# Kernel tuning notes

Hardware: AMD Instinct MI355X
Metric: run time of the kernel (lower is better)

Reference implementation:

```python
import jax, jax.numpy as jnp
import numpy as np

HIDDEN = 128
NUM_RADIAL = 16
NUM_DENSE = 3
OUT_DIM = 1
N_NODES = 50000
N_EDGES = 600000


def setup_inputs() -> dict:
    key = jax.random.key(0)
    ks = jax.random.split(key, 16)
    h = jax.random.normal(ks[0], (N_NODES, HIDDEN), dtype=jnp.float32)
    radial_basis = jax.random.normal(ks[1], (N_EDGES, NUM_RADIAL), dtype=jnp.float32)
    edge_index = jax.random.randint(ks[2], (2, N_EDGES), 0, N_NODES, dtype=jnp.int32)

    def lin(k, fan_in, fan_out):
        bound = 1.0 / np.sqrt(fan_in)
        kw, kb = jax.random.split(k)
        W = jax.random.uniform(kw, (fan_in, fan_out), minval=-bound, maxval=bound, dtype=jnp.float32)
        b = jax.random.uniform(kb, (fan_out,), minval=-bound, maxval=bound, dtype=jnp.float32)
        return W, b

    rW1, rb1 = lin(ks[3], NUM_RADIAL, HIDDEN)
    rW2, rb2 = lin(ks[4], HIDDEN, HIDDEN)
    dW, db = [], []
    for i in range(NUM_DENSE):
        W, b = lin(ks[5 + i], HIDDEN, HIDDEN)
        dW.append(W); db.append(b)
    oW, ob = lin(ks[10], HIDDEN, OUT_DIM)
    return {
        "h": h, "radial_basis": radial_basis, "edge_index": edge_index,
        "rW1": rW1, "rb1": rb1, "rW2": rW2, "rb2": rb2,
        "dW0": dW[0], "db0": db[0], "dW1": dW[1], "db1": db[1], "dW2": dW[2], "db2": db[2],
        "oW": oW, "ob": ob,
    }


def reference(h, radial_basis, edge_index, rW1, rb1, rW2, rb2,
              dW0, db0, dW1, db1, dW2, db2, oW, ob):
    src, dst = edge_index[0], edge_index[1]
    # radial_net: Linear -> SiLU -> Linear, output [n_edges, hidden]
    W = jax.nn.silu(radial_basis @ rW1 + rb1) @ rW2 + rb2
    # gather -> multiply -> scatter-add (message passing)
    h_edge = h[src] * W                      # [n_edges, hidden]
    x = jax.ops.segment_sum(h_edge, dst, num_segments=h.shape[0])  # [n_atoms, hidden]
    # dense layers
    for dw, dbias in ((dW0, db0), (dW1, db1), (dW2, db2)):
        x = jax.nn.silu(x @ dw + dbias)
    return x @ oW + ob                        # [n_atoms, output_dim]
```

## Files before the change

### kernel.cpp

```cpp
#include <hip/hip_runtime.h>

typedef short bf16x8 __attribute__((ext_vector_type(8)));
typedef float f32x4 __attribute__((ext_vector_type(4)));
typedef float f32x2 __attribute__((ext_vector_type(2)));
typedef unsigned int u32x4 __attribute__((ext_vector_type(4)));

__device__ __forceinline__ unsigned short f2bf(float f) {
  unsigned int u = __float_as_uint(f);
  u = (u + 0x7FFFu + ((u >> 16) & 1u)) >> 16;
  return (unsigned short)u;
}
__device__ __forceinline__ float bf2f(unsigned short u) {
  return __uint_as_float(((unsigned int)u) << 16);
}
__device__ __forceinline__ float silu_f(float v) {
  return v * (1.0f / (1.0f + __expf(-v)));
}
__device__ __forceinline__ unsigned int pkbf(float a, float b) {
  unsigned int r;
  asm("v_cvt_pk_bf16_f32 %0, %1, %2" : "=v"(r) : "v"(a), "v"(b));
  return r;
}
__device__ __forceinline__ void st2bf(char* base, int byA, int byB, float a, float b) {
  unsigned int p = pkbf(a, b);
  *(unsigned short*)(base + byA) = (unsigned short)p;
  *(unsigned short*)(base + byB) = (unsigned short)(p >> 16);
}

__global__ void k_prep(const float* __restrict__ rW1, const float* __restrict__ rb1,
                       const float* __restrict__ rW2, const float* __restrict__ dW0,
                       const float* __restrict__ dW1, const float* __restrict__ dW2,
                       unsigned short* __restrict__ wb) {
  int i = blockIdx.x * blockDim.x + threadIdx.x;
  if (i < 4096) {
    int j = i & 7, lane = (i >> 3) & 63, nt = i >> 9;
    int k = (lane >> 4) * 8 + j, n = nt * 16 + (lane & 15);
    float v = (k < 16) ? rW1[k * 128 + n] : (k == 16 ? rb1[n] : 0.0f);
    wb[i] = f2bf(v);
  } else if (i < 4096 + 4 * 16384) {
    int i2 = i - 4096, buf = i2 >> 14, r = i2 & 16383;
    int j = r & 7, lane = (r >> 3) & 63, g = r >> 9, kc = g & 3, nt = g >> 2;
    int k = kc * 32 + (lane >> 4) * 8 + j, n = nt * 16 + (lane & 15);
    const float* W = (buf == 0) ? rW2 : (buf == 1) ? dW0 : (buf == 2) ? dW1 : dW2;
    wb[4096 + buf * 16384 + r] = f2bf(W[k * 128 + n]);
  }
}

__global__ void k_hist(const int* __restrict__ ei, int* __restrict__ hist, int E) {
  int e = blockIdx.x * blockDim.x + threadIdx.x;
  if (e < E) atomicAdd(&hist[ei[E + e]], 1);
}

__global__ __launch_bounds__(1024) void k_scanA(const int* __restrict__ hist,
                                                int* __restrict__ part, int N) {
  __shared__ int red[1024];
  const int t = threadIdx.x;
  const int i = blockIdx.x * 1024 + t;
  red[t] = (i < N) ? hist[i] : 0;
  __syncthreads();
  for (int o = 512; o; o >>= 1) {
    if (t < o) red[t] += red[t + o];
    __syncthreads();
  }
  if (t == 0) part[blockIdx.x] = red[0];
}

__global__ __launch_bounds__(1024) void k_scanC(
    const int* __restrict__ hist, const int* __restrict__ part,
    int* __restrict__ row_start, int* __restrict__ bump, int N, int nb) {
  __shared__ int sh[1024];
  __shared__ int s_off;
  const int t = threadIdx.x;
  const int b = blockIdx.x;
  if (t < 64) {
    int p = (t < nb) ? part[t] : 0;
#pragma unroll
    for (int o = 1; o < 64; o <<= 1) {
      int u = __shfl_up(p, o);
      if (t >= o) p += u;
    }
    if (b == 0) {
      if (t == 0) s_off = 0;
    } else if (t == b - 1) {
      s_off = p;
    }
  }
  __syncthreads();
  const int i = b * 1024 + t;
  const int v = (i < N) ? hist[i] : 0;
  sh[t] = v;
  __syncthreads();
  for (int o = 1; o < 1024; o <<= 1) {
    int u = (t >= o) ? sh[t - o] : 0;
    __syncthreads();
    sh[t] += u;
    __syncthreads();
  }
  const int excl = s_off + sh[t] - v;
  if (i < N) {
    row_start[i] = excl;
    bump[i] = excl;
  } else if (i == N) {
    row_start[N] = excl;
  }
}

__global__ void k_pos(const int* __restrict__ ei, int* __restrict__ bump,
                      int* __restrict__ pos, int E) {
  int e = blockIdx.x * blockDim.x + threadIdx.x;
  if (e < E) pos[e] = atomicAdd(&bump[ei[E + e]], 1);
}

__global__ __launch_bounds__(256, 2) void k_edge2(
    const float* __restrict__ rb, const int* __restrict__ ei,
    const float* __restrict__ h, const unsigned short* __restrict__ B1,
    const unsigned short* __restrict__ B2, const float* __restrict__ rb2,
    const int* __restrict__ pos, unsigned short* __restrict__ Mbuf,
    int E, int ntiles) {
  const int lane = threadIdx.x & 63;
  const int wid = threadIdx.x >> 6;
  const int kg = lane >> 4;
  const int c15 = lane & 15;
  __shared__ __align__(16) unsigned short hid[64 * 128];

  bf16x8 b2f[8][4];
#pragma unroll
  for (int nt = 0; nt < 8; ++nt)
#pragma unroll
    for (int kc = 0; kc < 4; ++kc)
      b2f[nt][kc] = *(const bf16x8*)(B2 + (((nt * 4 + kc) * 64 + lane) << 3));

  float rb2r[8];
#pragma unroll
  for (int nt = 0; nt < 8; ++nt) rb2r[nt] = rb2[nt * 16 + c15];

  for (int t = blockIdx.x; t < ntiles; t += gridDim.x) {
    const int ebase = t * 64 + wid * 16;

    bf16x8 a1 = {};
    if (kg < 2) {
      const int e = ebase + c15;
      if (e < E) {
        const f32x4 v0 = __builtin_nontemporal_load((const f32x4*)(rb + (size_t)e * 16 + kg * 8));
        const f32x4 v1 = __builtin_nontemporal_load((const f32x4*)(rb + (size_t)e * 16 + kg * 8 + 4));
        unsigned int p0 = pkbf(v0[0], v0[1]), p1 = pkbf(v0[2], v0[3]);
        unsigned int p2 = pkbf(v1[0], v1[1]), p3 = pkbf(v1[2], v1[3]);
        a1[0] = (short)(p0 & 0xffff); a1[1] = (short)(p0 >> 16);
        a1[2] = (short)(p1 & 0xffff); a1[3] = (short)(p1 >> 16);
        a1[4] = (short)(p2 & 0xffff); a1[5] = (short)(p2 >> 16);
        a1[6] = (short)(p3 & 0xffff); a1[7] = (short)(p3 >> 16);
      }
    } else if (kg == 2) {
      a1[0] = (short)0x3F80;
    }

#pragma unroll
    for (int nt = 0; nt < 8; ++nt) {
      bf16x8 b1 = *(const bf16x8*)(B1 + ((nt * 64 + lane) << 3));
      f32x4 d1 = {};
      d1 = __builtin_amdgcn_mfma_f32_16x16x32_bf16(a1, b1, d1, 0, 0, 0);
#pragma unroll
      for (int r = 0; r < 4; r += 2) {
        const int row0 = wid * 16 + kg * 4 + r;
        const int row1 = row0 + 1;
        const int col2 = (nt * 16 + c15) * 2;
        st2bf((char*)hid,
              (row0 * 256 + col2) ^ ((row0 & 7) << 4),
              (row1 * 256 + col2) ^ ((row1 & 7) << 4),
              silu_f(d1[r]), silu_f(d1[r + 1]));
      }
    }

    const int arow = wid * 16 + c15;
    f32x4 acc[8] = {};
#pragma unroll
    for (int kc = 0; kc < 4; ++kc) {
      int byt = arow * 256 + (kc * 32 + kg * 8) * 2;
      byt ^= (arow & 7) << 4;
      const bf16x8 a2 = *(const bf16x8*)((const char*)hid + byt);
#pragma unroll
      for (int nt = 0; nt < 8; ++nt)
        acc[nt] = __builtin_amdgcn_mfma_f32_16x16x32_bf16(a2, b2f[nt][kc], acc[nt], 0, 0, 0);
    }

#pragma unroll
    for (int nt = 0; nt < 8; ++nt)
#pragma unroll
      for (int r = 0; r < 4; r += 2) {
        const int row0 = wid * 16 + kg * 4 + r;
        const int row1 = row0 + 1;
        const int col2 = (nt * 16 + c15) * 2;
        st2bf((char*)hid,
              (row0 * 256 + col2) ^ ((row0 & 7) << 4),
              (row1 * 256 + col2) ^ ((row1 & 7) << 4),
              acc[nt][r] + rb2r[nt], acc[nt][r + 1] + rb2r[nt]);
      }

#pragma unroll
    for (int pass = 0; pass < 2; ++pass) {
      const int ro = wid * 16 + pass * 8 + (lane >> 3);
      const int e = t * 64 + ro;
      if (e < E) {
        const int p = pos[e];
        const int s = ei[e];
        const int cg = (lane & 7) * 16;
        const int swz = (ro & 7) << 4;
        const int bas = ro * 256 + cg * 2;
        const bf16x8 w0 = *(const bf16x8*)((const char*)hid + (bas ^ swz));
        const bf16x8 w1 = *(const bf16x8*)((const char*)hid + ((bas + 16) ^ swz));
        const f32x4* hp = (const f32x4*)(h + (size_t)s * 128 + cg);
        const f32x4 h0 = hp[0], h1 = hp[1], h2 = hp[2], h3 = hp[3];
        u32x4 m0, m1;
        m0[0] = pkbf(bf2f((unsigned short)w0[0]) * h0[0], bf2f((unsigned short)w0[1]) * h0[1]);
        m0[1] = pkbf(bf2f((unsigned short)w0[2]) * h0[2], bf2f((unsigned short)w0[3]) * h0[3]);
        m0[2] = pkbf(bf2f((unsigned short)w0[4]) * h1[0], bf2f((unsigned short)w0[5]) * h1[1]);
        m0[3] = pkbf(bf2f((unsigned short)w0[6]) * h1[2], bf2f((unsigned short)w0[7]) * h1[3]);
        m1[0] = pkbf(bf2f((unsigned short)w1[0]) * h2[0], bf2f((unsigned short)w1[1]) * h2[1]);
        m1[1] = pkbf(bf2f((unsigned short)w1[2]) * h2[2], bf2f((unsigned short)w1[3]) * h2[3]);
        m1[2] = pkbf(bf2f((unsigned short)w1[4]) * h3[0], bf2f((unsigned short)w1[5]) * h3[1]);
        m1[3] = pkbf(bf2f((unsigned short)w1[6]) * h3[2], bf2f((unsigned short)w1[7]) * h3[3]);
        *(u32x4*)(Mbuf + (size_t)p * 128 + cg) = m0;
        *(u32x4*)(Mbuf + (size_t)p * 128 + cg + 8) = m1;
      }
    }
  }
}

__global__ __launch_bounds__(256) void k_gather2(
    const unsigned short* __restrict__ Mbuf, const int* __restrict__ row_start,
    float* __restrict__ x, int NN) {
  const int lane = threadIdx.x & 63;
  const int r4 = lane >> 4;
  const int c16 = lane & 15;
  const int wv = (int)((blockIdx.x * blockDim.x + threadIdx.x) >> 6);
  const int nw = (int)((gridDim.x * blockDim.x) >> 6);
  for (int n = wv; n < NN; n += nw) {
    const int b0 = row_start[n], b1 = row_start[n + 1];
    float sa[8] = {}, sb[8] = {};
    int j = b0 + r4;
    for (; j + 4 < b1; j += 8) {
      const bf16x8 va = *(const bf16x8*)(Mbuf + (size_t)j * 128 + c16 * 8);
      const bf16x8 vb = *(const bf16x8*)(Mbuf + (size_t)(j + 4) * 128 + c16 * 8);
#pragma unroll
      for (int k = 0; k < 8; ++k) {
        sa[k] += bf2f((unsigned short)va[k]);
        sb[k] += bf2f((unsigned short)vb[k]);
      }
    }
    if (j < b1) {
      const bf16x8 va = *(const bf16x8*)(Mbuf + (size_t)j * 128 + c16 * 8);
#pragma unroll
      for (int k = 0; k < 8; ++k) sa[k] += bf2f((unsigned short)va[k]);
    }
#pragma unroll
    for (int k = 0; k < 8; ++k) {
      float s = sa[k] + sb[k];
      s += __shfl_xor(s, 16);
      s += __shfl_xor(s, 32);
      sa[k] = s;
    }
    if (r4 == 0) {
      f32x4 o0 = {sa[0], sa[1], sa[2], sa[3]};
      f32x4 o1 = {sa[4], sa[5], sa[6], sa[7]};
      *(f32x4*)(x + (size_t)n * 128 + c16 * 8) = o0;
      *(f32x4*)(x + (size_t)n * 128 + c16 * 8 + 4) = o1;
    }
  }
}

__device__ __forceinline__ void dense_silu_layer(
    unsigned short* xt, const unsigned short* __restrict__ W,
    const float* __restrict__ bias, int wid, int kg, int c15, int lane) {
  const int arow = wid * 16 + c15;
  f32x4 acc[8] = {};
#pragma unroll
  for (int kc = 0; kc < 4; ++kc) {
    int byt = arow * 256 + (kc * 32 + kg * 8) * 2;
    byt ^= (arow & 7) << 4;
    const bf16x8 a2 = *(const bf16x8*)((const char*)xt + byt);
#pragma unroll
    for (int nt = 0; nt < 8; ++nt) {
      const bf16x8 bf = *(const bf16x8*)(W + (((nt * 4 + kc) * 64 + lane) << 3));
      acc[nt] = __builtin_amdgcn_mfma_f32_16x16x32_bf16(a2, bf, acc[nt], 0, 0, 0);
    }
  }
#pragma unroll
  for (int nt = 0; nt < 8; ++nt) {
    const float b = bias[nt * 16 + c15];
#pragma unroll
    for (int r = 0; r < 4; r += 2) {
      const int row0 = wid * 16 + kg * 4 + r;
      const int row1 = row0 + 1;
      const int col2 = (nt * 16 + c15) * 2;
      st2bf((char*)xt,
            (row0 * 256 + col2) ^ ((row0 & 7) << 4),
            (row1 * 256 + col2) ^ ((row1 & 7) << 4),
            silu_f(acc[nt][r] + b), silu_f(acc[nt][r + 1] + b));
    }
  }
}

__global__ __launch_bounds__(256) void k_tile(
    const float* __restrict__ x, const unsigned short* __restrict__ Dw,
    const float* __restrict__ db0, const float* __restrict__ db1,
    const float* __restrict__ db2, const float* __restrict__ oW,
    const float* __restrict__ ob, float* __restrict__ out, int NN, int tiles) {
  const int lane = threadIdx.x & 63;
  const int wid = threadIdx.x >> 6;
  const int kg = lane >> 4;
  const int c15 = lane & 15;
  __shared__ __align__(16) unsigned short xt[64 * 128];

  for (int t = blockIdx.x; t < tiles; t += gridDim.x) {
    const int nbase = t * 64 + wid * 16;

#pragma unroll
    for (int i = 0; i < 16; ++i) {
      const int n = nbase + i;
      const int row = wid * 16 + i;
      f32x2 v = {};
      if (n < NN) v = *(const f32x2*)(x + (size_t)n * 128 + lane * 2);
      const int byt = (row * 256 + lane * 4) ^ ((row & 7) << 4);
      *(unsigned int*)((char*)xt + byt) = pkbf(v[0], v[1]);
    }

    dense_silu_layer(xt, Dw, db0, wid, kg, c15, lane);
    dense_silu_layer(xt, Dw + 16384, db1, wid, kg, c15, lane);

    {
      const int arow = wid * 16 + c15;
      const unsigned short* W = Dw + 32768;
      f32x4 acc[8] = {};
#pragma unroll
      for (int kc = 0; kc < 4; ++kc) {
        int byt = arow * 256 + (kc * 32 + kg * 8) * 2;
        byt ^= (arow & 7) << 4;
        const bf16x8 a2 = *(const bf16x8*)((const char*)xt + byt);
#pragma unroll
        for (int nt = 0; nt < 8; ++nt) {
          const bf16x8 bf = *(const bf16x8*)(W + (((nt * 4 + kc) * 64 + lane) << 3));
          acc[nt] = __builtin_amdgcn_mfma_f32_16x16x32_bf16(a2, bf, acc[nt], 0, 0, 0);
        }
      }
      const float obv = ob[0];
#pragma unroll
      for (int r = 0; r < 4; ++r) {
        float p = 0.f;
#pragma unroll
        for (int nt = 0; nt < 8; ++nt) {
          const float b = db2[nt * 16 + c15];
          p += silu_f(acc[nt][r] + b) * oW[nt * 16 + c15];
        }
        p += __shfl_xor(p, 1);
        p += __shfl_xor(p, 2);
        p += __shfl_xor(p, 4);
        p += __shfl_xor(p, 8);
        const int n = nbase + kg * 4 + r;
        if (c15 == 0 && n < NN) out[n] = p + obv;
      }
    }
  }
}

__global__ __launch_bounds__(256, 2) void k_edge(
    const float* __restrict__ rb, const int* __restrict__ ei,
    const float* __restrict__ h, const unsigned short* __restrict__ B1,
    const unsigned short* __restrict__ B2, const float* __restrict__ rb2,
    float* __restrict__ x, int E, int ntiles) {
  const int lane = threadIdx.x & 63;
  const int wid = threadIdx.x >> 6;
  const int kg = lane >> 4;
  const int c15 = lane & 15;
  __shared__ __align__(16) unsigned short hid[64 * 128];

  bf16x8 b2f[8][4];
#pragma unroll
  for (int nt = 0; nt < 8; ++nt)
#pragma unroll
    for (int kc = 0; kc < 4; ++kc)
      b2f[nt][kc] = *(const bf16x8*)(B2 + (((nt * 4 + kc) * 64 + lane) << 3));

  float rb2r[8];
#pragma unroll
  for (int nt = 0; nt < 8; ++nt) rb2r[nt] = rb2[nt * 16 + c15];

  for (int t = blockIdx.x; t < ntiles; t += gridDim.x) {
    const int ebase = t * 64 + wid * 16;
    bf16x8 a1 = {};
    if (kg < 2) {
      const int e = ebase + c15;
      if (e < E) {
        const f32x4 v0 = *(const f32x4*)(rb + (size_t)e * 16 + kg * 8);
        const f32x4 v1 = *(const f32x4*)(rb + (size_t)e * 16 + kg * 8 + 4);
        a1[0] = (short)f2bf(v0[0]); a1[1] = (short)f2bf(v0[1]);
        a1[2] = (short)f2bf(v0[2]); a1[3] = (short)f2bf(v0[3]);
        a1[4] = (short)f2bf(v1[0]); a1[5] = (short)f2bf(v1[1]);
        a1[6] = (short)f2bf(v1[2]); a1[7] = (short)f2bf(v1[3]);
      }
    } else if (kg == 2) {
      a1[0] = (short)0x3F80;
    }
#pragma unroll
    for (int nt = 0; nt < 8; ++nt) {
      bf16x8 b1 = *(const bf16x8*)(B1 + ((nt * 64 + lane) << 3));
      f32x4 d1 = {};
      d1 = __builtin_amdgcn_mfma_f32_16x16x32_bf16(a1, b1, d1, 0, 0, 0);
#pragma unroll
      for (int r = 0; r < 4; ++r) {
        const int row = wid * 16 + kg * 4 + r;
        int byt = row * 256 + (nt * 16 + c15) * 2;
        byt ^= (row & 7) << 4;
        *(unsigned short*)((char*)hid + byt) = f2bf(silu_f(d1[r]));
      }
    }
    const int arow = wid * 16 + c15;
    f32x4 acc[8] = {};
#pragma unroll
    for (int kc = 0; kc < 4; ++kc) {
      int byt = arow * 256 + (kc * 32 + kg * 8) * 2;
      byt ^= (arow & 7) << 4;
      const bf16x8 a2 = *(const bf16x8*)((const char*)hid + byt);
#pragma unroll
      for (int nt = 0; nt < 8; ++nt)
        acc[nt] = __builtin_amdgcn_mfma_f32_16x16x32_bf16(a2, b2f[nt][kc], acc[nt], 0, 0, 0);
    }
#pragma unroll
    for (int r = 0; r < 4; ++r) {
      const int e = ebase + kg * 4 + r;
      if (e < E) {
        const int s = ei[e];
        const int d = ei[E + e];
#pragma unroll
        for (int nt = 0; nt < 8; ++nt) {
          const int col = nt * 16 + c15;
          const float w = acc[nt][r] + rb2r[nt];
          const float hv = h[(size_t)s * 128 + col];
          atomicAdd(x + (size_t)d * 128 + col, w * hv);
        }
      }
    }
  }
}

__global__ __launch_bounds__(256, 2) void k_dense(
    float* __restrict__ x, const unsigned short* __restrict__ Bw,
    const float* __restrict__ bias, int M) {
  const int lane = threadIdx.x & 63;
  const int wid = threadIdx.x >> 6;
  const int kg = lane >> 4;
  const int c15 = lane & 15;

  bf16x8 bf[8][4];
#pragma unroll
  for (int nt = 0; nt < 8; ++nt)
#pragma unroll
    for (int kc = 0; kc < 4; ++kc)
      bf[nt][kc] = *(const bf16x8*)(Bw + (((nt * 4 + kc) * 64 + lane) << 3));

  float br[8];
#pragma unroll
  for (int nt = 0; nt < 8; ++nt) br[nt] = bias[nt * 16 + c15];

  const int tiles = (M + 63) >> 6;
  for (int t = blockIdx.x; t < tiles; t += gridDim.x) {
    const int rbase = t * 64 + wid * 16;
    const int row = rbase + c15;
    bf16x8 a[4];
#pragma unroll
    for (int kc = 0; kc < 4; ++kc) {
      bf16x8 az = {};
      if (row < M) {
        const f32x4 v0 = *(const f32x4*)(x + (size_t)row * 128 + kc * 32 + kg * 8);
        const f32x4 v1 = *(const f32x4*)(x + (size_t)row * 128 + kc * 32 + kg * 8 + 4);
        az[0] = (short)f2bf(v0[0]); az[1] = (short)f2bf(v0[1]);
        az[2] = (short)f2bf(v0[2]); az[3] = (short)f2bf(v0[3]);
        az[4] = (short)f2bf(v1[0]); az[5] = (short)f2bf(v1[1]);
        az[6] = (short)f2bf(v1[2]); az[7] = (short)f2bf(v1[3]);
      }
      a[kc] = az;
    }
    f32x4 acc[8] = {};
#pragma unroll
    for (int kc = 0; kc < 4; ++kc)
#pragma unroll
      for (int nt = 0; nt < 8; ++nt)
        acc[nt] = __builtin_amdgcn_mfma_f32_16x16x32_bf16(a[kc], bf[nt][kc], acc[nt], 0, 0, 0);
#pragma unroll
    for (int r = 0; r < 4; ++r) {
      const int orow = rbase + kg * 4 + r;
      if (orow < M) {
#pragma unroll
        for (int nt = 0; nt < 8; ++nt)
          x[(size_t)orow * 128 + nt * 16 + c15] = silu_f(acc[nt][r] + br[nt]);
      }
    }
  }
}

__global__ void k_out(const float* __restrict__ x, const float* __restrict__ oW,
                      const float* __restrict__ ob, float* __restrict__ out, int M) {
  const int lane = threadIdx.x & 63;
  const int w = (int)((blockIdx.x * blockDim.x + threadIdx.x) >> 6);
  const int nw = (int)((gridDim.x * blockDim.x) >> 6);
  const float w0 = oW[lane], w1 = oW[64 + lane];
  const float obv = ob[0];
  for (int row = w; row < M; row += nw) {
    float a = x[(size_t)row * 128 + lane] * w0 + x[(size_t)row * 128 + 64 + lane] * w1;
#pragma unroll
    for (int m = 32; m; m >>= 1) a += __shfl_xor(a, m);
    if (lane == 0) out[row] = a + obv;
  }
}

extern "C" void kernel_launch(void* const* d_in, const int* in_sizes, int n_in,
                              void* d_out, int out_size, void* d_ws, size_t ws_size,
                              hipStream_t stream) {
  const float* h   = (const float*)d_in[0];
  const float* rb  = (const float*)d_in[1];
  const int*   ei  = (const int*)d_in[2];
  const float* rW1 = (const float*)d_in[3];
  const float* rb1 = (const float*)d_in[4];
  const float* rW2 = (const float*)d_in[5];
  const float* rb2 = (const float*)d_in[6];
  const float* dW0 = (const float*)d_in[7];
  const float* db0 = (const float*)d_in[8];
  const float* dW1 = (const float*)d_in[9];
  const float* db1 = (const float*)d_in[10];
  const float* dW2 = (const float*)d_in[11];
  const float* db2 = (const float*)d_in[12];
  const float* oW  = (const float*)d_in[13];
  const float* ob  = (const float*)d_in[14];

  const int NN = in_sizes[0] / 128;
  const int E  = in_sizes[1] / 16;

  char* base = (char*)d_ws;
  size_t off = 0;
  auto alloc = [&](size_t bytes) {
    char* p = base + off;
    off += (bytes + 255) & ~(size_t)255;
    return p;
  };
  float* x            = (float*)alloc((size_t)NN * 128 * 4);
  unsigned short* wb  = (unsigned short*)alloc((size_t)69632 * 2);
  int* row_start      = (int*)alloc((size_t)(NN + 1) * 4);
  int* hist           = (int*)alloc((size_t)NN * 4);
  int* bump           = (int*)alloc((size_t)NN * 4);
  int* part           = (int*)alloc((size_t)64 * 4);
  int* pos            = (int*)alloc((size_t)E * 4);
  unsigned short* Mb  = (unsigned short*)alloc((size_t)E * 256);
  const bool fits = off <= ws_size && NN <= 65535;

  k_prep<<<(69632 + 255) / 256, 256, 0, stream>>>(rW1, rb1, rW2, dW0, dW1, dW2, wb);

  const int ntiles = (E + 63) / 64;
  const int gE = (E + 255) / 256;

  if (fits) {
    hipMemsetAsync(hist, 0, (size_t)NN * 4, stream);
    k_hist<<<gE, 256, 0, stream>>>(ei, hist, E);
    k_scanA<<<64, 1024, 0, stream>>>(hist, part, NN);
    k_scanC<<<64, 1024, 0, stream>>>(hist, part, row_start, bump, NN, 64);
    k_pos<<<gE, 256, 0, stream>>>(ei, bump, pos, E);
    const int eg = ntiles < 2048 ? ntiles : 2048;
    k_edge2<<<eg, 256, 0, stream>>>(rb, ei, h, wb, wb + 4096, rb2, pos, Mb, E, ntiles);
    k_gather2<<<(NN + 3) / 4, 256, 0, stream>>>(Mb, row_start, x, NN);
    const int tiles = (NN + 63) / 64;
    k_tile<<<tiles, 256, 0, stream>>>(x, wb + 20480, db0, db1, db2,
                                      oW, ob, (float*)d_out, NN, tiles);
  } else {
    hipMemsetAsync(x, 0, (size_t)NN * 512, stream);
    const int eg = ntiles < 1024 ? ntiles : 1024;
    k_edge<<<eg, 256, 0, stream>>>(rb, ei, h, wb, wb + 4096, rb2, x, E, ntiles);
    k_dense<<<512, 256, 0, stream>>>(x, wb + 20480, db0, NN);
    k_dense<<<512, 256, 0, stream>>>(x, wb + 36864, db1, NN);
    k_dense<<<512, 256, 0, stream>>>(x, wb + 53248, db2, NN);
    k_out<<<512, 256, 0, stream>>>(x, oW, ob, (float*)d_out, NN);
  }
}
```

Baseline: 315.5 us.

## Sort edges by destination and reduce messages in-tile instead of via buffer

Edges are now sorted by destination into an (edge, src, dst) array, and the edge kernel processes the sorted slots. Messages are kept in shared memory and segment-reduced per tile, so only interior segments are written directly and tile-boundary segments use atomics into x. This removes the E×256-byte bf16 message buffer round trip and the separate gather kernel, at the cost of random reads of radial_basis by original edge id, a memset of x, and float atomics at segment boundaries. The grid is now one block per tile instead of a persistent loop, so B2 fragments are reloaded per tile.

```diff
diff --git a/kernel.cpp b/kernel.cpp
--- a/kernel.cpp
+++ b/kernel.cpp
@@ -67,7 +67,7 @@
 
 __global__ __launch_bounds__(1024) void k_scanC(
     const int* __restrict__ hist, const int* __restrict__ part,
-    int* __restrict__ row_start, int* __restrict__ bump, int N, int nb) {
+    int* __restrict__ bump, int N, int nb) {
   __shared__ int sh[1024];
   __shared__ int s_off;
   const int t = threadIdx.x;
@@ -96,32 +96,39 @@
     sh[t] += u;
     __syncthreads();
   }
-  const int excl = s_off + sh[t] - v;
-  if (i < N) {
-    row_start[i] = excl;
-    bump[i] = excl;
-  } else if (i == N) {
-    row_start[N] = excl;
-  }
-}
-
-__global__ void k_pos(const int* __restrict__ ei, int* __restrict__ bump,
-                      int* __restrict__ pos, int E) {
+  if (i < N) bump[i] = s_off + sh[t] - v;
+}
+
+__global__ void k_pos2(const int* __restrict__ ei, int* __restrict__ bump,
+                       int4* __restrict__ esd, int E) {
   int e = blockIdx.x * blockDim.x + threadIdx.x;
-  if (e < E) pos[e] = atomicAdd(&bump[ei[E + e]], 1);
-}
-
-__global__ __launch_bounds__(256, 2) void k_edge2(
-    const float* __restrict__ rb, const int* __restrict__ ei,
-    const float* __restrict__ h, const unsigned short* __restrict__ B1,
-    const unsigned short* __restrict__ B2, const float* __restrict__ rb2,
-    const int* __restrict__ pos, unsigned short* __restrict__ Mbuf,
-    int E, int ntiles) {
-  const int lane = threadIdx.x & 63;
-  const int wid = threadIdx.x >> 6;
+  if (e < E) {
+    const int s = ei[e];
+    const int d = ei[E + e];
+    const int p = atomicAdd(&bump[d], 1);
+    esd[p] = make_int4(e, s, d, 0);
+  }
+}
+
+__global__ __launch_bounds__(256, 2) void k_edge3(
+    const float* __restrict__ rb, const float* __restrict__ h,
+    const unsigned short* __restrict__ B1, const unsigned short* __restrict__ B2,
+    const float* __restrict__ rb2, const int4* __restrict__ esd,
+    float* __restrict__ x, int E) {
+  const int tid = threadIdx.x;
+  const int lane = tid & 63;
+  const int wid = tid >> 6;
   const int kg = lane >> 4;
   const int c15 = lane & 15;
   __shared__ __align__(16) unsigned short hid[64 * 128];
+  __shared__ int sdst[64];
+
+  const int tbase = blockIdx.x * 64;
+
+  if (tid < 64) {
+    const int slot = tbase + tid;
+    sdst[tid] = (slot < E) ? esd[slot].z : -1;
+  }
 
   bf16x8 b2f[8][4];
 #pragma unroll
@@ -134,137 +141,112 @@
 #pragma unroll
   for (int nt = 0; nt < 8; ++nt) rb2r[nt] = rb2[nt * 16 + c15];
 
-  for (int t = blockIdx.x; t < ntiles; t += gridDim.x) {
-    const int ebase = t * 64 + wid * 16;
-
-    bf16x8 a1 = {};
-    if (kg < 2) {
-      const int e = ebase + c15;
-      if (e < E) {
-        const f32x4 v0 = __builtin_nontemporal_load((const f32x4*)(rb + (size_t)e * 16 + kg * 8));
-        const f32x4 v1 = __builtin_nontemporal_load((const f32x4*)(rb + (size_t)e * 16 + kg * 8 + 4));
-        unsigned int p0 = pkbf(v0[0], v0[1]), p1 = pkbf(v0[2], v0[3]);
-        unsigned int p2 = pkbf(v1[0], v1[1]), p3 = pkbf(v1[2], v1[3]);
-        a1[0] = (short)(p0 & 0xffff); a1[1] = (short)(p0 >> 16);
-        a1[2] = (short)(p1 & 0xffff); a1[3] = (short)(p1 >> 16);
-        a1[4] = (short)(p2 & 0xffff); a1[5] = (short)(p2 >> 16);
-        a1[6] = (short)(p3 & 0xffff); a1[7] = (short)(p3 >> 16);
-      }
-    } else if (kg == 2) {
-      a1[0] = (short)0x3F80;
-    }
-
-#pragma unroll
-    for (int nt = 0; nt < 8; ++nt) {
-      bf16x8 b1 = *(const bf16x8*)(B1 + ((nt * 64 + lane) << 3));
-      f32x4 d1 = {};
-      d1 = __builtin_amdgcn_mfma_f32_16x16x32_bf16(a1, b1, d1, 0, 0, 0);
-#pragma unroll
-      for (int r = 0; r < 4; r += 2) {
-        const int row0 = wid * 16 + kg * 4 + r;
-        const int row1 = row0 + 1;
-        const int col2 = (nt * 16 + c15) * 2;
-        st2bf((char*)hid,
-              (row0 * 256 + col2) ^ ((row0 & 7) << 4),
-              (row1 * 256 + col2) ^ ((row1 & 7) << 4),
-              silu_f(d1[r]), silu_f(d1[r + 1]));
-      }
-    }
-
-    const int arow = wid * 16 + c15;
-    f32x4 acc[8] = {};
-#pragma unroll
-    for (int kc = 0; kc < 4; ++kc) {
-      int byt = arow * 256 + (kc * 32 + kg * 8) * 2;
-      byt ^= (arow & 7) << 4;
-      const bf16x8 a2 = *(const bf16x8*)((const char*)hid + byt);
-#pragma unroll
-      for (int nt = 0; nt < 8; ++nt)
-        acc[nt] = __builtin_amdgcn_mfma_f32_16x16x32_bf16(a2, b2f[nt][kc], acc[nt], 0, 0, 0);
-    }
-
+  bf16x8 a1 = {};
+  if (kg < 2) {
+    const int slot = tbase + wid * 16 + c15;
+    if (slot < E) {
+      const int eid = esd[slot].x;
+      const f32x4 v0 = __builtin_nontemporal_load((const f32x4*)(rb + (size_t)eid * 16 + kg * 8));
+      const f32x4 v1 = __builtin_nontemporal_load((const f32x4*)(rb + (size_t)eid * 16 + kg * 8 + 4));
+      unsigned int p0 = pkbf(v0[0], v0[1]), p1 = pkbf(v0[2], v0[3]);
+      unsigned int p2 = pkbf(v1[0], v1[1]), p3 = pkbf(v1[2], v1[3]);
+      a1[0] = (short)(p0 & 0xffff); a1[1] = (short)(p0 >> 16);
+      a1[2] = (short)(p1 & 0xffff); a1[3] = (short)(p1 >> 16);
+      a1[4] = (short)(p2 & 0xffff); a1[5] = (short)(p2 >> 16);
+      a1[6] = (short)(p3 & 0xffff); a1[7] = (short)(p3 >> 16);
+    }
+  } else if (kg == 2) {
+    a1[0] = (short)0x3F80;
+  }
+
+#pragma unroll
+  for (int nt = 0; nt < 8; ++nt) {
+    bf16x8 b1 = *(const bf16x8*)(B1 + ((nt * 64 + lane) << 3));
+    f32x4 d1 = {};
+    d1 = __builtin_amdgcn_mfma_f32_16x16x32_bf16(a1, b1, d1, 0, 0, 0);
+#pragma unroll
+    for (int r = 0; r < 4; r += 2) {
+      const int row0 = wid * 16 + kg * 4 + r;
+      const int row1 = row0 + 1;
+      const int col2 = (nt * 16 + c15) * 2;
+      st2bf((char*)hid,
+            (row0 * 256 + col2) ^ ((row0 & 7) << 4),
+            (row1 * 256 + col2) ^ ((row1 & 7) << 4),
+            silu_f(d1[r]), silu_f(d1[r + 1]));
+    }
+  }
+
+  const int arow = wid * 16 + c15;
+  f32x4 acc[8] = {};
+#pragma unroll
+  for (int kc = 0; kc < 4; ++kc) {
+    int byt = arow * 256 + (kc * 32 + kg * 8) * 2;
+    byt ^= (arow & 7) << 4;
+    const bf16x8 a2 = *(const bf16x8*)((const char*)hid + byt);
 #pragma unroll
     for (int nt = 0; nt < 8; ++nt)
-#pragma unroll
-      for (int r = 0; r < 4; r += 2) {
-        const int row0 = wid * 16 + kg * 4 + r;
-        const int row1 = row0 + 1;
-        const int col2 = (nt * 16 + c15) * 2;
-        st2bf((char*)hid,
-              (row0 * 256 + col2) ^ ((row0 & 7) << 4),
-              (row1 * 256 + col2) ^ ((row1 & 7) << 4),
-              acc[nt][r] + rb2r[nt], acc[nt][r + 1] + rb2r[nt]);
-      }
-
-#pragma unroll
-    for (int pass = 0; pass < 2; ++pass) {
-      const int ro = wid * 16 + pass * 8 + (lane >> 3);
-      const int e = t * 64 + ro;
-      if (e < E) {
-        const int p = pos[e];
-        const int s = ei[e];
-        const int cg = (lane & 7) * 16;
-        const int swz = (ro & 7) << 4;
-        const int bas = ro * 256 + cg * 2;
-        const bf16x8 w0 = *(const bf16x8*)((const char*)hid + (bas ^ swz));
-        const bf16x8 w1 = *(const bf16x8*)((const char*)hid + ((bas + 16) ^ swz));
-        const f32x4* hp = (const f32x4*)(h + (size_t)s * 128 + cg);
-        const f32x4 h0 = hp[0], h1 = hp[1], h2 = hp[2], h3 = hp[3];
-        u32x4 m0, m1;
-        m0[0] = pkbf(bf2f((unsigned short)w0[0]) * h0[0], bf2f((unsigned short)w0[1]) * h0[1]);
-        m0[1] = pkbf(bf2f((unsigned short)w0[2]) * h0[2], bf2f((unsigned short)w0[3]) * h0[3]);
-        m0[2] = pkbf(bf2f((unsigned short)w0[4]) * h1[0], bf2f((unsigned short)w0[5]) * h1[1]);
-        m0[3] = pkbf(bf2f((unsigned short)w0[6]) * h1[2], bf2f((unsigned short)w0[7]) * h1[3]);
-        m1[0] = pkbf(bf2f((unsigned short)w1[0]) * h2[0], bf2f((unsigned short)w1[1]) * h2[1]);
-        m1[1] = pkbf(bf2f((unsigned short)w1[2]) * h2[2], bf2f((unsigned short)w1[3]) * h2[3]);
-        m1[2] = pkbf(bf2f((unsigned short)w1[4]) * h3[0], bf2f((unsigned short)w1[5]) * h3[1]);
-        m1[3] = pkbf(bf2f((unsigned short)w1[6]) * h3[2], bf2f((unsigned short)w1[7]) * h3[3]);
-        *(u32x4*)(Mbuf + (size_t)p * 128 + cg) = m0;
-        *(u32x4*)(Mbuf + (size_t)p * 128 + cg + 8) = m1;
-      }
-    }
-  }
-}
-
-__global__ __launch_bounds__(256) void k_gather2(
-    const unsigned short* __restrict__ Mbuf, const int* __restrict__ row_start,
-    float* __restrict__ x, int NN) {
-  const int lane = threadIdx.x & 63;
-  const int r4 = lane >> 4;
-  const int c16 = lane & 15;
-  const int wv = (int)((blockIdx.x * blockDim.x + threadIdx.x) >> 6);
-  const int nw = (int)((gridDim.x * blockDim.x) >> 6);
-  for (int n = wv; n < NN; n += nw) {
-    const int b0 = row_start[n], b1 = row_start[n + 1];
-    float sa[8] = {}, sb[8] = {};
-    int j = b0 + r4;
-    for (; j + 4 < b1; j += 8) {
-      const bf16x8 va = *(const bf16x8*)(Mbuf + (size_t)j * 128 + c16 * 8);
-      const bf16x8 vb = *(const bf16x8*)(Mbuf + (size_t)(j + 4) * 128 + c16 * 8);
-#pragma unroll
-      for (int k = 0; k < 8; ++k) {
-        sa[k] += bf2f((unsigned short)va[k]);
-        sb[k] += bf2f((unsigned short)vb[k]);
-      }
-    }
-    if (j < b1) {
-      const bf16x8 va = *(const bf16x8*)(Mbuf + (size_t)j * 128 + c16 * 8);
-#pragma unroll
-      for (int k = 0; k < 8; ++k) sa[k] += bf2f((unsigned short)va[k]);
-    }
-#pragma unroll
-    for (int k = 0; k < 8; ++k) {
-      float s = sa[k] + sb[k];
-      s += __shfl_xor(s, 16);
-      s += __shfl_xor(s, 32);
-      sa[k] = s;
-    }
-    if (r4 == 0) {
-      f32x4 o0 = {sa[0], sa[1], sa[2], sa[3]};
-      f32x4 o1 = {sa[4], sa[5], sa[6], sa[7]};
-      *(f32x4*)(x + (size_t)n * 128 + c16 * 8) = o0;
-      *(f32x4*)(x + (size_t)n * 128 + c16 * 8 + 4) = o1;
-    }
+      acc[nt] = __builtin_amdgcn_mfma_f32_16x16x32_bf16(a2, b2f[nt][kc], acc[nt], 0, 0, 0);
+  }
+
+#pragma unroll
+  for (int nt = 0; nt < 8; ++nt)
+#pragma unroll
+    for (int r = 0; r < 4; r += 2) {
+      const int row0 = wid * 16 + kg * 4 + r;
+      const int row1 = row0 + 1;
+      const int col2 = (nt * 16 + c15) * 2;
+      st2bf((char*)hid,
+            (row0 * 256 + col2) ^ ((row0 & 7) << 4),
+            (row1 * 256 + col2) ^ ((row1 & 7) << 4),
+            acc[nt][r] + rb2r[nt], acc[nt][r + 1] + rb2r[nt]);
+    }
+
+#pragma unroll
+  for (int pass = 0; pass < 2; ++pass) {
+    const int ro = wid * 16 + pass * 8 + (lane >> 3);
+    const int slot = tbase + ro;
+    if (slot < E) {
+      const int s = esd[slot].y;
+      const int cg = (lane & 7) * 16;
+      const int swz = (ro & 7) << 4;
+      const int bas = ro * 256 + cg * 2;
+      const bf16x8 w0 = *(const bf16x8*)((const char*)hid + (bas ^ swz));
+      const bf16x8 w1 = *(const bf16x8*)((const char*)hid + ((bas + 16) ^ swz));
+      const f32x4* hp = (const f32x4*)(h + (size_t)s * 128 + cg);
+      const f32x4 h0 = hp[0], h1 = hp[1], h2 = hp[2], h3 = hp[3];
+      u32x4 m0, m1;
+      m0[0] = pkbf(bf2f((unsigned short)w0[0]) * h0[0], bf2f((unsigned short)w0[1]) * h0[1]);
+      m0[1] = pkbf(bf2f((unsigned short)w0[2]) * h0[2], bf2f((unsigned short)w0[3]) * h0[3]);
+      m0[2] = pkbf(bf2f((unsigned short)w0[4]) * h1[0], bf2f((unsigned short)w0[5]) * h1[1]);
+      m0[3] = pkbf(bf2f((unsigned short)w0[6]) * h1[2], bf2f((unsigned short)w0[7]) * h1[3]);
+      m1[0] = pkbf(bf2f((unsigned short)w1[0]) * h2[0], bf2f((unsigned short)w1[1]) * h2[1]);
+      m1[1] = pkbf(bf2f((unsigned short)w1[2]) * h2[2], bf2f((unsigned short)w1[3]) * h2[3]);
+      m1[2] = pkbf(bf2f((unsigned short)w1[4]) * h3[0], bf2f((unsigned short)w1[5]) * h3[1]);
+      m1[3] = pkbf(bf2f((unsigned short)w1[6]) * h3[2], bf2f((unsigned short)w1[7]) * h3[3]);
+      *(u32x4*)((char*)hid + (bas ^ swz)) = m0;
+      *(u32x4*)((char*)hid + ((bas + 16) ^ swz)) = m1;
+    }
+  }
+
+  __syncthreads();
+
+  {
+    const int col = tid & 127;
+    const int r0 = (tid >> 7) << 5;
+    float a = 0.f;
+    int prev = sdst[r0];
+    int segstart = r0;
+    for (int row = r0; row < r0 + 32; ++row) {
+      const int d = sdst[row];
+      if (d != prev) {
+        float* xp = x + (size_t)prev * 128 + col;
+        if (segstart == r0) atomicAdd(xp, a); else *xp = a;
+        a = 0.f; prev = d; segstart = row;
+      }
+      const int byt = (row * 256 + col * 2) ^ ((row & 7) << 4);
+      a += bf2f(*(const unsigned short*)((const char*)hid + byt));
+    }
+    if (prev >= 0) atomicAdd(x + (size_t)prev * 128 + col, a);
   }
 }
 
@@ -543,28 +525,26 @@
   };
   float* x            = (float*)alloc((size_t)NN * 128 * 4);
   unsigned short* wb  = (unsigned short*)alloc((size_t)69632 * 2);
-  int* row_start      = (int*)alloc((size_t)(NN + 1) * 4);
   int* hist           = (int*)alloc((size_t)NN * 4);
   int* bump           = (int*)alloc((size_t)NN * 4);
   int* part           = (int*)alloc((size_t)64 * 4);
-  int* pos            = (int*)alloc((size_t)E * 4);
-  unsigned short* Mb  = (unsigned short*)alloc((size_t)E * 256);
+  int4* esd           = (int4*)alloc((size_t)E * 16);
   const bool fits = off <= ws_size && NN <= 65535;
 
   k_prep<<<(69632 + 255) / 256, 256, 0, stream>>>(rW1, rb1, rW2, dW0, dW1, dW2, wb);
 
   const int ntiles = (E + 63) / 64;
   const int gE = (E + 255) / 256;
+  const int nb = (NN + 1023) / 1024;
 
   if (fits) {
     hipMemsetAsync(hist, 0, (size_t)NN * 4, stream);
+    hipMemsetAsync(x, 0, (size_t)NN * 512, stream);
     k_hist<<<gE, 256, 0, stream>>>(ei, hist, E);
-    k_scanA<<<64, 1024, 0, stream>>>(hist, part, NN);
-    k_scanC<<<64, 1024, 0, stream>>>(hist, part, row_start, bump, NN, 64);
-    k_pos<<<gE, 256, 0, stream>>>(ei, bump, pos, E);
-    const int eg = ntiles < 2048 ? ntiles : 2048;
-    k_edge2<<<eg, 256, 0, stream>>>(rb, ei, h, wb, wb + 4096, rb2, pos, Mb, E, ntiles);
-    k_gather2<<<(NN + 3) / 4, 256, 0, stream>>>(Mb, row_start, x, NN);
+    k_scanA<<<nb, 1024, 0, stream>>>(hist, part, NN);
+    k_scanC<<<nb, 1024, 0, stream>>>(hist, part, bump, NN, nb);
+    k_pos2<<<gE, 256, 0, stream>>>(ei, bump, esd, E);
+    k_edge3<<<ntiles, 256, 0, stream>>>(rb, h, wb, wb + 4096, rb2, esd, x, E);
     const int tiles = (NN + 63) / 64;
     k_tile<<<tiles, 256, 0, stream>>>(x, wb + 20480, db0, db1, db2,
                                       oW, ob, (float*)d_out, NN, tiles);
```

Result: slower. 364.7 us (+15.6%).

## Fuse segment gather into dense-tile kernel and fold hist memset into prep

Applied to the files above, without the earlier changes.

Merges the CSR gather-sum kernel into the dense-layer tile kernel, so each 512-thread block sums messages for 128 nodes directly into shared memory as bf16. This drops the fp32 x round-trip through global memory and one kernel launch. It also zeroes the histogram inside k_prep instead of a separate memset and sizes the scan grids from NN. In exchange, the gather now processes two nodes per wave with divergent lengths and adds block-wide syncs before the MFMA layers.

```diff
diff --git a/kernel.cpp b/kernel.cpp
--- a/kernel.cpp
+++ b/kernel.cpp
@@ -30,7 +30,8 @@
 __global__ void k_prep(const float* __restrict__ rW1, const float* __restrict__ rb1,
                        const float* __restrict__ rW2, const float* __restrict__ dW0,
                        const float* __restrict__ dW1, const float* __restrict__ dW2,
-                       unsigned short* __restrict__ wb) {
+                       unsigned short* __restrict__ wb, int* __restrict__ hist,
+                       int nzero) {
   int i = blockIdx.x * blockDim.x + threadIdx.x;
   if (i < 4096) {
     int j = i & 7, lane = (i >> 3) & 63, nt = i >> 9;
@@ -43,6 +44,8 @@
     int k = kc * 32 + (lane >> 4) * 8 + j, n = nt * 16 + (lane & 15);
     const float* W = (buf == 0) ? rW2 : (buf == 1) ? dW0 : (buf == 2) ? dW1 : dW2;
     wb[4096 + buf * 16384 + r] = f2bf(W[k * 128 + n]);
+  } else if (i - 69632 < nzero) {
+    hist[i - 69632] = 0;
   }
 }
 
@@ -226,48 +229,6 @@
   }
 }
 
-__global__ __launch_bounds__(256) void k_gather2(
-    const unsigned short* __restrict__ Mbuf, const int* __restrict__ row_start,
-    float* __restrict__ x, int NN) {
-  const int lane = threadIdx.x & 63;
-  const int r4 = lane >> 4;
-  const int c16 = lane & 15;
-  const int wv = (int)((blockIdx.x * blockDim.x + threadIdx.x) >> 6);
-  const int nw = (int)((gridDim.x * blockDim.x) >> 6);
-  for (int n = wv; n < NN; n += nw) {
-    const int b0 = row_start[n], b1 = row_start[n + 1];
-    float sa[8] = {}, sb[8] = {};
-    int j = b0 + r4;
-    for (; j + 4 < b1; j += 8) {
-      const bf16x8 va = *(const bf16x8*)(Mbuf + (size_t)j * 128 + c16 * 8);
-      const bf16x8 vb = *(const bf16x8*)(Mbuf + (size_t)(j + 4) * 128 + c16 * 8);
-#pragma unroll
-      for (int k = 0; k < 8; ++k) {
-        sa[k] += bf2f((unsigned short)va[k]);
-        sb[k] += bf2f((unsigned short)vb[k]);
-      }
-    }
-    if (j < b1) {
-      const bf16x8 va = *(const bf16x8*)(Mbuf + (size_t)j * 128 + c16 * 8);
-#pragma unroll
-      for (int k = 0; k < 8; ++k) sa[k] += bf2f((unsigned short)va[k]);
-    }
-#pragma unroll
-    for (int k = 0; k < 8; ++k) {
-      float s = sa[k] + sb[k];
-      s += __shfl_xor(s, 16);
-      s += __shfl_xor(s, 32);
-      sa[k] = s;
-    }
-    if (r4 == 0) {
-      f32x4 o0 = {sa[0], sa[1], sa[2], sa[3]};
-      f32x4 o1 = {sa[4], sa[5], sa[6], sa[7]};
-      *(f32x4*)(x + (size_t)n * 128 + c16 * 8) = o0;
-      *(f32x4*)(x + (size_t)n * 128 + c16 * 8 + 4) = o1;
-    }
-  }
-}
-
 __device__ __forceinline__ void dense_silu_layer(
     unsigned short* xt, const unsigned short* __restrict__ W,
     const float* __restrict__ bias, int wid, int kg, int c15, int lane) {
@@ -300,29 +261,77 @@
   }
 }
 
-__global__ __launch_bounds__(256) void k_tile(
-    const float* __restrict__ x, const unsigned short* __restrict__ Dw,
-    const float* __restrict__ db0, const float* __restrict__ db1,
-    const float* __restrict__ db2, const float* __restrict__ oW,
-    const float* __restrict__ ob, float* __restrict__ out, int NN, int tiles) {
-  const int lane = threadIdx.x & 63;
-  const int wid = threadIdx.x >> 6;
+__global__ __launch_bounds__(512) void k_gtile(
+    const unsigned short* __restrict__ Mbuf, const int* __restrict__ row_start,
+    const unsigned short* __restrict__ Dw, const float* __restrict__ db0,
+    const float* __restrict__ db1, const float* __restrict__ db2,
+    const float* __restrict__ oW, const float* __restrict__ ob,
+    float* __restrict__ out, int NN, int tiles) {
+  const int tid = threadIdx.x;
+  const int lane = tid & 63;
+  const int wid = tid >> 6;
   const int kg = lane >> 4;
   const int c15 = lane & 15;
-  __shared__ __align__(16) unsigned short xt[64 * 128];
+  __shared__ __align__(16) unsigned short xt[128 * 128];
 
   for (int t = blockIdx.x; t < tiles; t += gridDim.x) {
-    const int nbase = t * 64 + wid * 16;
-
-#pragma unroll
-    for (int i = 0; i < 16; ++i) {
-      const int n = nbase + i;
-      const int row = wid * 16 + i;
-      f32x2 v = {};
-      if (n < NN) v = *(const f32x2*)(x + (size_t)n * 128 + lane * 2);
-      const int byt = (row * 256 + lane * 4) ^ ((row & 7) << 4);
-      *(unsigned int*)((char*)xt + byt) = pkbf(v[0], v[1]);
-    }
+    if (t != (int)blockIdx.x) __syncthreads();
+    const int rbase = wid * 16;
+    const int nbase = t * 128 + rbase;
+
+    for (int i = 0; i < 16; i += 2) {
+      const int nA = nbase + i, nB = nbase + i + 1;
+      int a0 = 0, a1 = 0, b0 = 0, b1 = 0;
+      if (nA < NN) { a0 = row_start[nA]; a1 = row_start[nA + 1]; }
+      if (nB < NN) { b0 = row_start[nB]; b1 = row_start[nB + 1]; }
+      const int lenA = a1 - a0, lenB = b1 - b0;
+      const int maxlen = lenA > lenB ? lenA : lenB;
+      float sa[8] = {}, sb[8] = {};
+      for (int off = kg; off < maxlen; off += 4) {
+        if (off < lenA) {
+          const bf16x8 v = *(const bf16x8*)(Mbuf + (size_t)(a0 + off) * 128 + c15 * 8);
+#pragma unroll
+          for (int k = 0; k < 8; ++k) sa[k] += bf2f((unsigned short)v[k]);
+        }
+        if (off < lenB) {
+          const bf16x8 v = *(const bf16x8*)(Mbuf + (size_t)(b0 + off) * 128 + c15 * 8);
+#pragma unroll
+          for (int k = 0; k < 8; ++k) sb[k] += bf2f((unsigned short)v[k]);
+        }
+      }
+#pragma unroll
+      for (int k = 0; k < 8; ++k) {
+        float s = sa[k];
+        s += __shfl_xor(s, 16);
+        s += __shfl_xor(s, 32);
+        sa[k] = s;
+        float q = sb[k];
+        q += __shfl_xor(q, 16);
+        q += __shfl_xor(q, 32);
+        sb[k] = q;
+      }
+      if (kg == 0) {
+        if (nA < NN) {
+          const int row = rbase + i;
+          u32x4 w;
+          w[0] = pkbf(sa[0], sa[1]); w[1] = pkbf(sa[2], sa[3]);
+          w[2] = pkbf(sa[4], sa[5]); w[3] = pkbf(sa[6], sa[7]);
+          const int byt = (row * 256 + c15 * 16) ^ ((row & 7) << 4);
+          *(u32x4*)((char*)xt + byt) = w;
+        }
+      } else if (kg == 1) {
+        if (nB < NN) {
+          const int row = rbase + i + 1;
+          u32x4 w;
+          w[0] = pkbf(sb[0], sb[1]); w[1] = pkbf(sb[2], sb[3]);
+          w[2] = pkbf(sb[4], sb[5]); w[3] = pkbf(sb[6], sb[7]);
+          const int byt = (row * 256 + c15 * 16) ^ ((row & 7) << 4);
+          *(u32x4*)((char*)xt + byt) = w;
+        }
+      }
+    }
+
+    __syncthreads();
 
     dense_silu_layer(xt, Dw, db0, wid, kg, c15, lane);
     dense_silu_layer(xt, Dw + 16384, db1, wid, kg, c15, lane);
@@ -551,24 +560,25 @@
   unsigned short* Mb  = (unsigned short*)alloc((size_t)E * 256);
   const bool fits = off <= ws_size && NN <= 65535;
 
-  k_prep<<<(69632 + 255) / 256, 256, 0, stream>>>(rW1, rb1, rW2, dW0, dW1, dW2, wb);
-
   const int ntiles = (E + 63) / 64;
   const int gE = (E + 255) / 256;
+  const int nb = (NN + 1023) / 1024;
 
   if (fits) {
-    hipMemsetAsync(hist, 0, (size_t)NN * 4, stream);
+    k_prep<<<(69632 + NN + 255) / 256, 256, 0, stream>>>(rW1, rb1, rW2, dW0, dW1,
+                                                         dW2, wb, hist, NN);
     k_hist<<<gE, 256, 0, stream>>>(ei, hist, E);
-    k_scanA<<<64, 1024, 0, stream>>>(hist, part, NN);
-    k_scanC<<<64, 1024, 0, stream>>>(hist, part, row_start, bump, NN, 64);
+    k_scanA<<<nb, 1024, 0, stream>>>(hist, part, NN);
+    k_scanC<<<nb, 1024, 0, stream>>>(hist, part, row_start, bump, NN, nb);
     k_pos<<<gE, 256, 0, stream>>>(ei, bump, pos, E);
     const int eg = ntiles < 2048 ? ntiles : 2048;
     k_edge2<<<eg, 256, 0, stream>>>(rb, ei, h, wb, wb + 4096, rb2, pos, Mb, E, ntiles);
-    k_gather2<<<(NN + 3) / 4, 256, 0, stream>>>(Mb, row_start, x, NN);
-    const int tiles = (NN + 63) / 64;
-    k_tile<<<tiles, 256, 0, stream>>>(x, wb + 20480, db0, db1, db2,
-                                      oW, ob, (float*)d_out, NN, tiles);
+    const int gt = (NN + 127) / 128;
+    k_gtile<<<gt, 512, 0, stream>>>(Mb, row_start, wb + 20480, db0, db1, db2,
+                                    oW, ob, (float*)d_out, NN, gt);
   } else {
+    k_prep<<<(69632 + 255) / 256, 256, 0, stream>>>(rW1, rb1, rW2, dW0, dW1,
+                                                    dW2, wb, hist, 0);
     hipMemsetAsync(x, 0, (size_t)NN * 512, stream);
     const int eg = ntiles < 1024 ? ntiles : 1024;
     k_edge<<<eg, 256, 0, stream>>>(rb, ei, h, wb, wb + 4096, rb2, x, E, ntiles);
```

After: 306.2 us. 2.9% less time.
